# Optimization experiments

Measured on AMD Instinct MI355X. Metric: run time of the kernel, lower is better.

Reference implementation:

```python
import jax, jax.numpy as jnp
import numpy as np
from jax import lax

DIM = 192
PATCH = 8


def conv1x1(x, w):
    # x: [b,c,h,w], w: [o,c] (1x1 conv, no bias)
    return jnp.einsum('bchw,oc->bohw', x, w)


def dwconv(x, w, b, pad):
    # depthwise conv, w: [C,1,kh,kw], groups = C
    y = lax.conv_general_dilated(
        x, w, window_strides=(1, 1), padding=((pad, pad), (pad, pad)),
        dimension_numbers=('NCHW', 'OIHW', 'NCHW'),
        feature_group_count=x.shape[1])
    return y + b[None, :, None, None]


def to_patches(x, p):
    b, c, h, w = x.shape
    ph = (-h) % p
    pw = (-w) % p
    x = jnp.pad(x, ((0, 0), (0, 0), (0, ph), (0, pw)))
    H, W = h + ph, w + pw
    x = x.reshape(b, c, H // p, p, W // p, p)
    return x.transpose(0, 1, 2, 4, 3, 5)  # b c nh nw p p


def from_patches(x, h, w):
    b, c, nh, nw, p, _ = x.shape
    x = x.transpose(0, 1, 2, 4, 3, 5).reshape(b, c, nh * p, nw * p)
    return x[:, :, :h, :w]


def setup_inputs() -> dict:
    key = jax.random.key(0)
    ks = jax.random.split(key, 8)
    b, c, h, w = 4, DIM, 256, 256
    x = jax.random.normal(ks[0], (b, c, h, w), jnp.float32)
    wq = jax.random.normal(ks[1], (c, c), jnp.float32) * 0.02
    w_qdw = jax.random.normal(ks[2], (c, 1, 3, 3), jnp.float32) * 0.1
    b_qdw = jnp.zeros((c,), jnp.float32)
    wkv = jax.random.normal(ks[3], (2 * c, c), jnp.float32) * 0.02
    w_kvdw = jax.random.normal(ks[4], (2 * c, 1, 7, 7), jnp.float32) * 0.05
    b_kvdw = jnp.zeros((2 * c,), jnp.float32)
    ln_w = jnp.ones((c,), jnp.float32)
    ln_b = jnp.zeros((c,), jnp.float32)
    w_proj = jax.random.normal(ks[5], (c, c), jnp.float32) * 0.02
    b_proj = jnp.zeros((c,), jnp.float32)
    return {'x': x, 'wq': wq, 'w_qdw': w_qdw, 'b_qdw': b_qdw,
            'wkv': wkv, 'w_kvdw': w_kvdw, 'b_kvdw': b_kvdw,
            'ln_w': ln_w, 'ln_b': ln_b, 'w_proj': w_proj, 'b_proj': b_proj}


def reference(x, wq, w_qdw, b_qdw, wkv, w_kvdw, b_kvdw, ln_w, ln_b, w_proj, b_proj):
    b, c, h, w = x.shape
    p = PATCH
    q = dwconv(conv1x1(x, wq), w_qdw, b_qdw, pad=1)
    kv = dwconv(conv1x1(x, wkv), w_kvdw, b_kvdw, pad=3)
    k, v = kv[:, :c], kv[:, c:]
    qp = to_patches(q, p).astype(jnp.float32)
    kp = to_patches(k, p).astype(jnp.float32)
    out = jnp.fft.irfft2(jnp.fft.rfft2(qp) * jnp.fft.rfft2(kp), s=(p, p))
    out = from_patches(out, h, w)
    # WithBias LayerNorm over channel dim (channels-last LN in original)
    mu = out.mean(axis=1, keepdims=True)
    var = out.var(axis=1, keepdims=True)
    out = (out - mu) / jnp.sqrt(var + 1e-5)
    out = out * ln_w[None, :, None, None] + ln_b[None, :, None, None]
    out = out * v
    out = conv1x1(out, w_proj) + b_proj[None, :, None, None]
    return out
```

## Files before the change

kernel.cpp:

```cpp
#include <hip/hip_runtime.h>
#include <hip/hip_bf16.h>

#define HW 65536
#define IMG 256
static constexpr int CDIM = 192;

typedef __attribute__((ext_vector_type(8))) short short8;
typedef __attribute__((ext_vector_type(4))) short s16x4;
typedef __attribute__((ext_vector_type(4))) float f32x4;

static __device__ __forceinline__ float b2f(unsigned short u) {
    union { unsigned u; float f; } t; t.u = ((unsigned)u) << 16; return t.f;
}
static __device__ __forceinline__ unsigned short f2bu(float f) {
    __hip_bfloat16 h = __float2bfloat16(f);
    return *reinterpret_cast<unsigned short*>(&h);
}

__global__ void pack_weights(const float* __restrict__ wq,
                             const float* __restrict__ wkv,
                             const float* __restrict__ wp,
                             __hip_bfloat16* __restrict__ Wqkv,
                             __hip_bfloat16* __restrict__ Wp) {
    int i = blockIdx.x * 256 + threadIdx.x;
    if (i < 36864) Wqkv[i] = __float2bfloat16(wq[i]);
    else if (i < 110592) Wqkv[i] = __float2bfloat16(wkv[i - 36864]);
    else if (i < 147456) Wp[i - 110592] = __float2bfloat16(wp[i - 110592]);
}

__global__ void transpose_cvt(const float* __restrict__ x,
                              __hip_bfloat16* __restrict__ xT) {
    __shared__ float tile[32][33];
    const int p0 = blockIdx.x * 32, c0 = blockIdx.y * 32;
    const int tx = threadIdx.x & 31, ty = threadIdx.x >> 5;
#pragma unroll
    for (int r = 0; r < 4; r++)
        tile[ty + r * 8][tx] = x[(size_t)(c0 + ty + r * 8) * HW + p0 + tx];
    __syncthreads();
#pragma unroll
    for (int r = 0; r < 4; r++)
        xT[(size_t)(p0 + ty + r * 8) * 192 + c0 + tx] =
            __float2bfloat16(tile[tx][ty + r * 8]);
}

__global__ void gemm_bf16(const __hip_bfloat16* __restrict__ A,
                          const __hip_bfloat16* __restrict__ Bt,
                          __hip_bfloat16* __restrict__ Y) {
    __shared__ short Bs[128][200];
    const int tid = threadIdx.x;
    const int wid = tid >> 6, lane = tid & 63;
    const int mBase = blockIdx.x * 64, nBase = blockIdx.y * 128;

#pragma unroll
    for (int l = 0; l < 12; l++) {
        int ch = tid + l * 256;
        int row = ch / 24, cc = ch % 24;
        short8 v = *(const short8*)(Bt + (size_t)(nBase + row) * 192 + cc * 8);
        *(short8*)&Bs[row][cc * 8] = v;
    }
    __syncthreads();

    const int lr = lane & 15, lg = lane >> 4;
    const __hip_bfloat16* Ab = A + (size_t)(mBase + wid * 16 + lr) * 192 + lg * 8;
    f32x4 acc[8];
#pragma unroll
    for (int f = 0; f < 8; f++) acc[f] = (f32x4){0.f, 0.f, 0.f, 0.f};

#pragma unroll
    for (int ks = 0; ks < 6; ks++) {
        short8 af = *(const short8*)(Ab + ks * 32);
#pragma unroll
        for (int f = 0; f < 8; f++) {
            short8 bfr = *(const short8*)&Bs[f * 16 + lr][ks * 32 + lg * 8];
            acc[f] = __builtin_amdgcn_mfma_f32_16x16x32_bf16(af, bfr, acc[f], 0, 0, 0);
        }
    }

    const int mrow = mBase + wid * 16 + lg * 4;
#pragma unroll
    for (int f = 0; f < 8; f++) {
        int n = nBase + f * 16 + lr;
#pragma unroll
        for (int r = 0; r < 4; r++)
            Y[(size_t)(mrow + r) * HW + n] = __float2bfloat16(acc[f][r]);
    }
}

__global__ __launch_bounds__(256) void dwconv7_v4(
    const __hip_bfloat16* __restrict__ in,
    const float* __restrict__ wdw,
    const float* __restrict__ bias,
    __hip_bfloat16* __restrict__ out) {
    __shared__ unsigned short tile[70][136];
    const int c = blockIdx.y;
    const int x0 = (blockIdx.x & 1) * 128;
    const int y0 = (blockIdx.x >> 1) * 64;
    const __hip_bfloat16* src = in + (size_t)c * HW;

    float w49[49];
#pragma unroll
    for (int i = 0; i < 49; i++) w49[i] = wdw[c * 49 + i];
    const float bval = bias[c];

#pragma unroll
    for (int l = 0; l < 5; l++) {
        int idx = threadIdx.x + l * 256;
        if (idx < 70 * 17) {
            int r = idx / 17, cs = idx - r * 17;
            int gy = y0 + r - 3;
            int gxb = x0 + cs * 8 - 3;
            if ((unsigned)gy < IMG && gxb >= 0 && gxb + 8 <= IMG) {
                *(short8*)&tile[r][cs * 8] =
                    *(const short8*)(src + gy * IMG + gxb);
            } else {
#pragma unroll
                for (int e = 0; e < 8; e++) {
                    int gx = gxb + e;
                    unsigned short val = 0;
                    if ((unsigned)gy < IMG && (unsigned)gx < IMG)
                        val = *(const unsigned short*)(src + gy * IMG + gx);
                    tile[r][cs * 8 + e] = val;
                }
            }
        }
    }
    __syncthreads();

    const int tx4 = (threadIdx.x & 31) * 4;
    const int gy8 = (threadIdx.x >> 5) * 8;
    float acc[8][4];
#pragma unroll
    for (int j = 0; j < 8; j++)
#pragma unroll
        for (int xx = 0; xx < 4; xx++) acc[j][xx] = bval;

#pragma unroll
    for (int rr = 0; rr < 14; rr++) {
        const unsigned short* rowp = &tile[gy8 + rr][tx4];
        s16x4 a0 = *(const s16x4*)(rowp);
        s16x4 a1 = *(const s16x4*)(rowp + 4);
        s16x4 a2 = *(const s16x4*)(rowp + 8);
        float win[12];
#pragma unroll
        for (int e = 0; e < 4; e++) {
            win[e]     = b2f((unsigned short)a0[e]);
            win[e + 4] = b2f((unsigned short)a1[e]);
            win[e + 8] = b2f((unsigned short)a2[e]);
        }
#pragma unroll
        for (int j = 0; j < 8; j++) {
            const int ky = rr - j;
            if (ky >= 0 && ky < 7) {
#pragma unroll
                for (int kx = 0; kx < 7; kx++)
#pragma unroll
                    for (int xx = 0; xx < 4; xx++)
                        acc[j][xx] += win[xx + kx] * w49[ky * 7 + kx];
            }
        }
    }

    __hip_bfloat16* dst = out + (size_t)c * HW + (size_t)(y0 + gy8) * IMG + x0 + tx4;
#pragma unroll
    for (int j = 0; j < 8; j++) {
        union { unsigned short h[4]; unsigned long long u; } ob;
#pragma unroll
        for (int xx = 0; xx < 4; xx++) ob.h[xx] = f2bu(acc[j][xx]);
        *(unsigned long long*)(dst + (size_t)j * IMG) = ob.u;
    }
}

__global__ __launch_bounds__(256) void circ_qfused(
    const __hip_bfloat16* __restrict__ q0,
    const __hip_bfloat16* __restrict__ kbuf,
    const float* __restrict__ w_qdw, const float* __restrict__ b_qdw,
    __hip_bfloat16* __restrict__ sout) {
    __shared__ float qs[10][264];
    __shared__ float qP[32][68];
    __shared__ float kP[32][68];
    const int c = blockIdx.y, ph = blockIdx.x;
    const int y0 = ph * 8;
    const __hip_bfloat16* qsrc = q0 + (size_t)c * HW;
    const __hip_bfloat16* ksrc = kbuf + (size_t)c * HW;

    for (int idx = threadIdx.x; idx < 10 * 258; idx += 256) {
        int ly = idx / 258, lx = idx - ly * 258;
        int gy = y0 + ly - 1, gx = lx - 1;
        float v = 0.f;
        if ((unsigned)gy < IMG && (unsigned)gx < IMG)
            v = b2f(*(const unsigned short*)(qsrc + gy * IMG + gx));
        qs[ly][lx] = v;
    }
    {
        const int x = threadIdx.x;
#pragma unroll
        for (int a = 0; a < 8; a++) {
            float v = b2f(*(const unsigned short*)(ksrc + (y0 + a) * IMG + x));
            kP[x >> 3][a * 8 + (x & 7)] = v;
        }
    }
    __syncthreads();

    {
        const int x = threadIdx.x;
        float w9[9];
#pragma unroll
        for (int i = 0; i < 9; i++) w9[i] = w_qdw[c * 9 + i];
        float accq[8];
#pragma unroll
        for (int j = 0; j < 8; j++) accq[j] = b_qdw[c];
#pragma unroll
        for (int kx = 0; kx < 3; kx++)
#pragma unroll
            for (int yy = 0; yy < 10; yy++) {
                float vv = qs[yy][x + kx];
#pragma unroll
                for (int j = 0; j < 8; j++) {
                    int ky = yy - j;
                    if (ky >= 0 && ky < 3) accq[j] += vv * w9[ky * 3 + kx];
                }
            }
#pragma unroll
        for (int j = 0; j < 8; j++) qP[x >> 3][j * 8 + (x & 7)] = accq[j];
    }
    __syncthreads();

    const int i = threadIdx.x >> 5, pw = threadIdx.x & 31;
    float qv[8][8];
#pragma unroll
    for (int a = 0; a < 8; a++) {
        f32x4 u0 = *(const f32x4*)&qP[pw][a * 8];
        f32x4 u1 = *(const f32x4*)&qP[pw][a * 8 + 4];
        qv[a][0] = u0[0]; qv[a][1] = u0[1]; qv[a][2] = u0[2]; qv[a][3] = u0[3];
        qv[a][4] = u1[0]; qv[a][5] = u1[1]; qv[a][6] = u1[2]; qv[a][7] = u1[3];
    }
    float acc[8];
#pragma unroll
    for (int j = 0; j < 8; j++) acc[j] = 0.f;
#pragma unroll
    for (int a = 0; a < 8; a++) {
        const int r = (i - a + 8) & 7;
        f32x4 k0v = *(const f32x4*)&kP[pw][r * 8];
        f32x4 k1v = *(const f32x4*)&kP[pw][r * 8 + 4];
        float kr[8] = {k0v[0], k0v[1], k0v[2], k0v[3],
                       k1v[0], k1v[1], k1v[2], k1v[3]};
#pragma unroll
        for (int b = 0; b < 8; b++)
#pragma unroll
            for (int j = 0; j < 8; j++)
                acc[j] += qv[a][b] * kr[(j - b + 8) & 7];
    }
    union { unsigned short h[8]; short8 s8; } ob;
#pragma unroll
    for (int j = 0; j < 8; j++) ob.h[j] = f2bu(acc[j]);
    *(short8*)(sout + (size_t)c * HW + (size_t)(y0 + i) * IMG + pw * 8) = ob.s8;
}

__global__ __launch_bounds__(256, 2) void gemm_proj_ln(
    const __hip_bfloat16* __restrict__ Wp,
    const __hip_bfloat16* __restrict__ s,
    const __hip_bfloat16* __restrict__ v,
    const float* __restrict__ ln_w, const float* __restrict__ ln_b,
    const float* __restrict__ bias,
    float* __restrict__ Y) {
    __shared__ short Bs[128][200];
    __shared__ float red[2][2][128];
    __shared__ float muA[128], rsA[128];
    const int tid = threadIdx.x;
    const int p0 = blockIdx.x * 128;
    const int px = tid & 127, h = tid >> 7;
    const unsigned short* sp = (const unsigned short*)s;

    float sum = 0.f, sq = 0.f;
#pragma unroll 4
    for (int l = 0; l < 48; l++) {
        int c = h * 96 + l * 2;
        unsigned short ua = sp[(size_t)c * HW + p0 + px];
        unsigned short ub = sp[(size_t)(c + 1) * HW + p0 + px];
        float a = b2f(ua), b = b2f(ub);
        sum += a + b;
        sq += a * a + b * b;
        *(unsigned*)&Bs[px][c] = (unsigned)ua | ((unsigned)ub << 16);
    }
    red[h][0][px] = sum;
    red[h][1][px] = sq;
    __syncthreads();
    if (tid < 128) {
        float sm = red[0][0][tid] + red[1][0][tid];
        float sQ = red[0][1][tid] + red[1][1][tid];
        float mu = sm * (1.f / 192.f);
        float var = sQ * (1.f / 192.f) - mu * mu;
        muA[tid] = mu;
        rsA[tid] = rsqrtf(var + 1e-5f);
    }
    __syncthreads();

    const float mu = muA[px], rs = rsA[px];
#pragma unroll 4
    for (int l = 0; l < 48; l++) {
        int c = h * 96 + l * 2;
        unsigned pr = *(unsigned*)&Bs[px][c];
        float a = b2f((unsigned short)pr);
        float b = b2f((unsigned short)(pr >> 16));
        float va = b2f(*(const unsigned short*)(v + (size_t)c * HW + p0 + px));
        float vb = b2f(*(const unsigned short*)(v + (size_t)(c + 1) * HW + p0 + px));
        a = ((a - mu) * rs * ln_w[c] + ln_b[c]) * va;
        b = ((b - mu) * rs * ln_w[c + 1] + ln_b[c + 1]) * vb;
        *(unsigned*)&Bs[px][c] = (unsigned)f2bu(a) | ((unsigned)f2bu(b) << 16);
    }
    __syncthreads();

    const int wid = tid >> 6, lane = tid & 63;
    const int lr = lane & 15, lg = lane >> 4;
    f32x4 acc[3][8];
#pragma unroll
    for (int mf = 0; mf < 3; mf++)
#pragma unroll
        for (int f = 0; f < 8; f++) acc[mf][f] = (f32x4){0.f, 0.f, 0.f, 0.f};

#pragma unroll
    for (int ks = 0; ks < 6; ks++) {
        short8 bfr[8];
#pragma unroll
        for (int f = 0; f < 8; f++)
            bfr[f] = *(const short8*)&Bs[f * 16 + lr][ks * 32 + lg * 8];
#pragma unroll
        for (int mf = 0; mf < 3; mf++) {
            int mrow = wid * 48 + mf * 16 + lr;
            short8 af = *(const short8*)(Wp + (size_t)mrow * 192 + ks * 32 + lg * 8);
#pragma unroll
            for (int f = 0; f < 8; f++)
                acc[mf][f] = __builtin_amdgcn_mfma_f32_16x16x32_bf16(af, bfr[f], acc[mf][f], 0, 0, 0);
        }
    }

#pragma unroll
    for (int mf = 0; mf < 3; mf++) {
        int m0 = wid * 48 + mf * 16 + lg * 4;
#pragma unroll
        for (int f = 0; f < 8; f++) {
            int n = p0 + f * 16 + lr;
#pragma unroll
            for (int r = 0; r < 4; r++)
                Y[(size_t)(m0 + r) * HW + n] = acc[mf][f][r] + bias[m0 + r];
        }
    }
}

extern "C" void kernel_launch(void* const* d_in, const int* in_sizes, int n_in,
                              void* d_out, int out_size, void* d_ws, size_t ws_size,
                              hipStream_t stream) {
    const float* x      = (const float*)d_in[0];
    const float* wq     = (const float*)d_in[1];
    const float* w_qdw  = (const float*)d_in[2];
    const float* b_qdw  = (const float*)d_in[3];
    const float* wkv    = (const float*)d_in[4];
    const float* w_kvdw = (const float*)d_in[5];
    const float* b_kvdw = (const float*)d_in[6];
    const float* ln_w   = (const float*)d_in[7];
    const float* ln_b   = (const float*)d_in[8];
    const float* w_proj = (const float*)d_in[9];
    const float* b_proj = (const float*)d_in[10];
    float* out = (float*)d_out;
    char* ws = (char*)d_ws;

    __hip_bfloat16* qkv0  = (__hip_bfloat16*)(ws + 0);
    __hip_bfloat16* kvbuf = (__hip_bfloat16*)(ws + 75497472ull);
    __hip_bfloat16* sbuf  = (__hip_bfloat16*)(ws + 125829120ull);
    __hip_bfloat16* xT    = (__hip_bfloat16*)(ws + 150994944ull);
    __hip_bfloat16* Wqkv  = (__hip_bfloat16*)(ws + 176160768ull);
    __hip_bfloat16* Wp    = Wqkv + 110592;

    pack_weights<<<576, 256, 0, stream>>>(wq, wkv, w_proj, Wqkv, Wp);

    for (int b = 0; b < 4; b++) {
        const float* xb = x + (size_t)b * CDIM * HW;
        transpose_cvt<<<dim3(HW / 32, 6), 256, 0, stream>>>(xb, xT);
        gemm_bf16<<<dim3(9, HW / 128), 256, 0, stream>>>(Wqkv, xT, qkv0);
        dwconv7_v4<<<dim3(8, 384), 256, 0, stream>>>(qkv0 + (size_t)192 * HW,
                                                     w_kvdw, b_kvdw, kvbuf);
        circ_qfused<<<dim3(32, 192), 256, 0, stream>>>(qkv0, kvbuf,
                                                       w_qdw, b_qdw, sbuf);
        gemm_proj_ln<<<HW / 128, 256, 0, stream>>>(Wp, sbuf,
                                                   kvbuf + (size_t)192 * HW,
                                                   ln_w, ln_b, b_proj,
                                                   out + (size_t)b * CDIM * HW);
    }
}
```

Before: 715.3 us.

## Fuse input transpose/convert into QKV GEMM and vectorize circ_qfused loads

Removes the separate transpose_cvt kernel: the QKV GEMM now reads fp32 x in channel-major layout directly, converts to bf16 and packs channel pairs into its shared B tile. This drops a full write and read of the bf16 transposed intermediate per batch, plus one launch. The trade-off is that each of the 9 M-blocks now re-reads fp32 X, which doubles bytes per read compared with bf16, and the read is coalesced across pixels only. The circ_qfused halo and k-patch loads are also vectorized to 16-byte bf16 loads with an offset shared layout and explicit zeroing of the border columns.

```diff
diff --git a/kernel.cpp b/kernel.cpp
--- a/kernel.cpp
+++ b/kernel.cpp
@@ -28,35 +28,21 @@
     else if (i < 147456) Wp[i - 110592] = __float2bfloat16(wp[i - 110592]);
 }
 
-__global__ void transpose_cvt(const float* __restrict__ x,
-                              __hip_bfloat16* __restrict__ xT) {
-    __shared__ float tile[32][33];
-    const int p0 = blockIdx.x * 32, c0 = blockIdx.y * 32;
-    const int tx = threadIdx.x & 31, ty = threadIdx.x >> 5;
-#pragma unroll
-    for (int r = 0; r < 4; r++)
-        tile[ty + r * 8][tx] = x[(size_t)(c0 + ty + r * 8) * HW + p0 + tx];
-    __syncthreads();
-#pragma unroll
-    for (int r = 0; r < 4; r++)
-        xT[(size_t)(p0 + ty + r * 8) * 192 + c0 + tx] =
-            __float2bfloat16(tile[tx][ty + r * 8]);
-}
-
-__global__ void gemm_bf16(const __hip_bfloat16* __restrict__ A,
-                          const __hip_bfloat16* __restrict__ Bt,
-                          __hip_bfloat16* __restrict__ Y) {
+__global__ void gemm_bf16_x(const __hip_bfloat16* __restrict__ A,
+                            const float* __restrict__ X,
+                            __hip_bfloat16* __restrict__ Y) {
     __shared__ short Bs[128][200];
     const int tid = threadIdx.x;
     const int wid = tid >> 6, lane = tid & 63;
     const int mBase = blockIdx.x * 64, nBase = blockIdx.y * 128;
-
-#pragma unroll
-    for (int l = 0; l < 12; l++) {
-        int ch = tid + l * 256;
-        int row = ch / 24, cc = ch % 24;
-        short8 v = *(const short8*)(Bt + (size_t)(nBase + row) * 192 + cc * 8);
-        *(short8*)&Bs[row][cc * 8] = v;
+    const int px = tid & 127, h = tid >> 7;
+
+#pragma unroll 4
+    for (int l = 0; l < 48; l++) {
+        int c = h * 96 + l * 2;
+        float a = X[(size_t)c * HW + nBase + px];
+        float b = X[(size_t)(c + 1) * HW + nBase + px];
+        *(unsigned*)&Bs[px][c] = (unsigned)f2bu(a) | ((unsigned)f2bu(b) << 16);
     }
     __syncthreads();
 
@@ -183,21 +169,39 @@
     const __hip_bfloat16* qsrc = q0 + (size_t)c * HW;
     const __hip_bfloat16* ksrc = kbuf + (size_t)c * HW;
 
-    for (int idx = threadIdx.x; idx < 10 * 258; idx += 256) {
-        int ly = idx / 258, lx = idx - ly * 258;
-        int gy = y0 + ly - 1, gx = lx - 1;
-        float v = 0.f;
-        if ((unsigned)gy < IMG && (unsigned)gx < IMG)
-            v = b2f(*(const unsigned short*)(qsrc + gy * IMG + gx));
-        qs[ly][lx] = v;
+    for (int t = threadIdx.x; t < 340; t += 256) {
+        if (t < 320) {
+            int r = t >> 5, ch = t & 31;
+            int gy = y0 + r - 1;
+            f32x4 lo = (f32x4){0.f, 0.f, 0.f, 0.f};
+            f32x4 hi = (f32x4){0.f, 0.f, 0.f, 0.f};
+            if ((unsigned)gy < IMG) {
+                short8 v = *(const short8*)(qsrc + gy * IMG + ch * 8);
+#pragma unroll
+                for (int e = 0; e < 4; e++) {
+                    lo[e] = b2f((unsigned short)v[e]);
+                    hi[e] = b2f((unsigned short)v[4 + e]);
+                }
+            }
+            *(f32x4*)&qs[r][4 + ch * 8] = lo;
+            *(f32x4*)&qs[r][8 + ch * 8] = hi;
+        } else {
+            int e = t - 320;
+            int r = e >> 1, s = e & 1;
+            qs[r][s ? 260 : 3] = 0.f;
+        }
     }
     {
-        const int x = threadIdx.x;
-#pragma unroll
-        for (int a = 0; a < 8; a++) {
-            float v = b2f(*(const unsigned short*)(ksrc + (y0 + a) * IMG + x));
-            kP[x >> 3][a * 8 + (x & 7)] = v;
-        }
+        int a = threadIdx.x >> 5, ch = threadIdx.x & 31;
+        short8 v = *(const short8*)(ksrc + (y0 + a) * IMG + ch * 8);
+        f32x4 lo, hi;
+#pragma unroll
+        for (int e = 0; e < 4; e++) {
+            lo[e] = b2f((unsigned short)v[e]);
+            hi[e] = b2f((unsigned short)v[4 + e]);
+        }
+        *(f32x4*)&kP[ch][a * 8] = lo;
+        *(f32x4*)&kP[ch][a * 8 + 4] = hi;
     }
     __syncthreads();
 
@@ -213,7 +217,7 @@
         for (int kx = 0; kx < 3; kx++)
 #pragma unroll
             for (int yy = 0; yy < 10; yy++) {
-                float vv = qs[yy][x + kx];
+                float vv = qs[yy][x + kx + 3];
 #pragma unroll
                 for (int j = 0; j < 8; j++) {
                     int ky = yy - j;
@@ -367,16 +371,14 @@
     __hip_bfloat16* qkv0  = (__hip_bfloat16*)(ws + 0);
     __hip_bfloat16* kvbuf = (__hip_bfloat16*)(ws + 75497472ull);
     __hip_bfloat16* sbuf  = (__hip_bfloat16*)(ws + 125829120ull);
-    __hip_bfloat16* xT    = (__hip_bfloat16*)(ws + 150994944ull);
-    __hip_bfloat16* Wqkv  = (__hip_bfloat16*)(ws + 176160768ull);
+    __hip_bfloat16* Wqkv  = (__hip_bfloat16*)(ws + 150994944ull);
     __hip_bfloat16* Wp    = Wqkv + 110592;
 
     pack_weights<<<576, 256, 0, stream>>>(wq, wkv, w_proj, Wqkv, Wp);
 
     for (int b = 0; b < 4; b++) {
         const float* xb = x + (size_t)b * CDIM * HW;
-        transpose_cvt<<<dim3(HW / 32, 6), 256, 0, stream>>>(xb, xT);
-        gemm_bf16<<<dim3(9, HW / 128), 256, 0, stream>>>(Wqkv, xT, qkv0);
+        gemm_bf16_x<<<dim3(9, HW / 128), 256, 0, stream>>>(Wqkv, xb, qkv0);
         dwconv7_v4<<<dim3(8, 384), 256, 0, stream>>>(qkv0 + (size_t)192 * HW,
                                                      w_kvdw, b_kvdw, kvbuf);
         circ_qfused<<<dim3(32, 192), 256, 0, stream>>>(qkv0, kvbuf,
```

Result: no change. 727.5 us (+1.7%).
